# Performance work log

Hardware: AMD Instinct MI355X
Metric: run time of the kernel (lower is better)

The kernel has to match this reference:

```python
import jax, jax.numpy as jnp
import numpy as np

N = 50000      # nodes
E = 800000     # edges (before self-loops)
NFEAT = 128
NHID = 32
H = 8
NCLASS = 47
NEG_SLOPE = 0.2  # PyG GATv2Conv default


def gatv2_layer(x, src, dst, Wl, Wr, att, b, n):
    """One GATv2Conv layer (concat over heads). att: [H, C]."""
    h, c = att.shape
    xl = (x @ Wl).reshape(n, h, c)  # source transform (lin_l)
    xr = (x @ Wr).reshape(n, h, c)  # target transform (lin_r)
    e = jax.nn.leaky_relu(xl[src] + xr[dst], NEG_SLOPE)   # [E, H, C]
    logits = jnp.einsum('ehc,hc->eh', e, att)             # [E, H]
    # segment softmax over incoming edges of each target node
    m = jax.ops.segment_max(logits, dst, num_segments=n)  # [N, H]
    alpha = jnp.exp(logits - m[dst])
    denom = jax.ops.segment_sum(alpha, dst, num_segments=n)
    alpha = alpha / (denom[dst] + 1e-16)
    msg = xl[src] * alpha[:, :, None]                     # [E, H, C]
    out = jax.ops.segment_sum(msg, dst, num_segments=n)   # [N, H, C]
    return out.reshape(n, h * c) + b


def setup_inputs():
    key = jax.random.key(0)
    ks = jax.random.split(key, 16)
    s = 0.1
    x = jax.random.normal(ks[0], (N, NFEAT), jnp.float32)
    edge_index = jax.random.randint(ks[1], (2, E), 0, N)
    HID = H * NHID  # 256
    params = dict(
        Wl0=jax.random.normal(ks[2], (NFEAT, HID), jnp.float32) * s,
        Wr0=jax.random.normal(ks[3], (NFEAT, HID), jnp.float32) * s,
        a0=jax.random.normal(ks[4], (H, NHID), jnp.float32) * s,
        b0=jnp.zeros((HID,), jnp.float32),
        Wl1=jax.random.normal(ks[5], (HID, HID), jnp.float32) * s,
        Wr1=jax.random.normal(ks[6], (HID, HID), jnp.float32) * s,
        a1=jax.random.normal(ks[7], (H, NHID), jnp.float32) * s,
        b1=jnp.zeros((HID,), jnp.float32),
        Wl2=jax.random.normal(ks[8], (HID, NCLASS), jnp.float32) * s,
        Wr2=jax.random.normal(ks[9], (HID, NCLASS), jnp.float32) * s,
        a2=jax.random.normal(ks[10], (1, NCLASS), jnp.float32) * s,
        b2=jnp.zeros((NCLASS,), jnp.float32),
    )
    return {"x": x, "edge_index": edge_index, **params}


def reference(x, edge_index, Wl0, Wr0, a0, b0, Wl1, Wr1, a1, b1, Wl2, Wr2, a2, b2):
    n = x.shape[0]
    # PyG GATv2Conv adds self-loops by default
    loops = jnp.arange(n, dtype=edge_index.dtype)
    src = jnp.concatenate([edge_index[0], loops])
    dst = jnp.concatenate([edge_index[1], loops])
    h = gatv2_layer(x, src, dst, Wl0, Wr0, a0, b0, n)
    h = jax.nn.elu(h)
    h = gatv2_layer(h, src, dst, Wl1, Wr1, a1, b1, n)
    h = jax.nn.elu(h)
    h = gatv2_layer(h, src, dst, Wl2, Wr2, a2, b2, n)
    return jax.nn.log_softmax(h, axis=-1)
```

## Files before the change

kernel.cpp:

```cpp
#include <hip/hip_runtime.h>
#include <cmath>


#define NFEAT 128
#define HID 256
#define NCLS 47
#define L2PAD 64

typedef __attribute__((ext_vector_type(8))) short bf16x8;
typedef __attribute__((ext_vector_type(4))) float f32x4;
typedef __attribute__((ext_vector_type(2))) float f32x2;

__device__ __forceinline__ unsigned short f2b(float f) {
  unsigned int u = __builtin_bit_cast(unsigned int, f);
  u += 0x7FFFu + ((u >> 16) & 1u);
  return (unsigned short)(u >> 16);
}
__device__ __forceinline__ float b2f(unsigned short s) {
  return __builtin_bit_cast(float, (unsigned int)s << 16);
}
__device__ __forceinline__ f32x2 b2f2(unsigned int u) {
  return (f32x2){__builtin_bit_cast(float, u << 16),
                 __builtin_bit_cast(float, u & 0xFFFF0000u)};
}

__device__ __forceinline__ void glds16(const unsigned short* g, unsigned short* l) {
  __builtin_amdgcn_global_load_lds(
      (const __attribute__((address_space(1))) unsigned int*)g,
      (__attribute__((address_space(3))) unsigned int*)l, 16, 0, 0);
}

__global__ void k_cast_bf16(const float* __restrict__ in,
                            unsigned short* __restrict__ out, int n4) {
  int i = blockIdx.x * blockDim.x + threadIdx.x;
  if (i < n4) {
    float4 v = reinterpret_cast<const float4*>(in)[i];
    ushort4 o = {f2b(v.x), f2b(v.y), f2b(v.z), f2b(v.w)};
    reinterpret_cast<ushort4*>(out)[i] = o;
  }
}

struct WtArgs {
  const float* W[6];
  unsigned short* WT[6];
  int K[6], M[6], off[6], total;
};
__global__ void k_wt_all(WtArgs a) {
  int i = blockIdx.x * blockDim.x + threadIdx.x;
  if (i >= a.total) return;
  int s = 0;
  #pragma unroll
  for (int j = 1; j < 6; ++j) if (i >= a.off[j]) s = j;
  int jj = i - a.off[s];
  int K = a.K[s], M = a.M[s];
  int m = jj / K, k = jj - m * K;
  a.WT[s][jj] = (m < M) ? f2b(a.W[s][(size_t)k * M + m]) : (unsigned short)0;
}

__global__ void k_pad_att(const float* __restrict__ a, float* __restrict__ out48) {
  int i = threadIdx.x;
  if (i < 48) out48[i] = (i < NCLS) ? a[i] : 0.f;
}

__global__ void k_init_deg(int* __restrict__ deg, int n) {
  int i = blockIdx.x * blockDim.x + threadIdx.x;
  if (i < n) deg[i] = 1;
}

__global__ void k_count(const int* __restrict__ dst, int* __restrict__ deg, int e) {
  int i = blockIdx.x * blockDim.x + threadIdx.x;
  if (i < e) atomicAdd(&deg[dst[i]], 1);
}

__global__ __launch_bounds__(256) void k_bsum(const int* __restrict__ deg,
                                              int* __restrict__ bsum, int n) {
  int t = threadIdx.x;
  int base = blockIdx.x * 1024 + t * 4;
  int s = 0;
  if (base + 3 < n) {
    int4 v = *reinterpret_cast<const int4*>(deg + base);
    s = v.x + v.y + v.z + v.w;
  } else {
    for (int j = 0; j < 4; ++j) { int i = base + j; if (i < n) s += deg[i]; }
  }
  #pragma unroll
  for (int off = 1; off < 64; off <<= 1) s += __shfl_xor(s, off, 64);
  __shared__ int wsum[4];
  if ((t & 63) == 0) wsum[t >> 6] = s;
  __syncthreads();
  if (t == 0) bsum[blockIdx.x] = wsum[0] + wsum[1] + wsum[2] + wsum[3];
}

__global__ void k_scanb(int* __restrict__ bsum, int nb) {
  int lane = threadIdx.x;
  int v = (lane < nb) ? bsum[lane] : 0;
  #pragma unroll
  for (int off = 1; off < 64; off <<= 1) {
    int u = __shfl_up(v, off, 64);
    if (lane >= off) v += u;
  }
  if (lane < nb) bsum[lane] = v;
}

__global__ __launch_bounds__(256) void k_scanfinal(const int* __restrict__ deg,
                                                   const int* __restrict__ bscan,
                                                   int* __restrict__ rowptr, int n) {
  int t = threadIdx.x, b = blockIdx.x;
  int base = b * 1024 + t * 4;
  int v0 = 0, v1 = 0, v2 = 0, v3 = 0;
  if (base + 3 < n) {
    int4 v = *reinterpret_cast<const int4*>(deg + base);
    v0 = v.x; v1 = v.y; v2 = v.z; v3 = v.w;
  } else {
    if (base < n) v0 = deg[base];
    if (base + 1 < n) v1 = deg[base + 1];
    if (base + 2 < n) v2 = deg[base + 2];
    if (base + 3 < n) v3 = deg[base + 3];
  }
  int s = v0 + v1 + v2 + v3;
  int incl = s;
  #pragma unroll
  for (int off = 1; off < 64; off <<= 1) {
    int u = __shfl_up(incl, off, 64);
    if ((t & 63) >= off) incl += u;
  }
  __shared__ int wsum[4];
  int w = t >> 6, l = t & 63;
  if (l == 63) wsum[w] = incl;
  __syncthreads();
  int woff = 0;
  for (int j = 0; j < w; ++j) woff += wsum[j];
  int excl = incl - s + woff;
  int boff = (b == 0) ? 0 : bscan[b - 1];
  int p = boff + excl;
  if (base < n)     rowptr[base + 1] = p + v0;
  if (base + 1 < n) rowptr[base + 2] = p + v0 + v1;
  if (base + 2 < n) rowptr[base + 3] = p + v0 + v1 + v2;
  if (base + 3 < n) rowptr[base + 4] = p + v0 + v1 + v2 + v3;
  if (b == 0 && t == 0) rowptr[0] = 0;
}

__global__ void k_init_csr(const int* __restrict__ rowptr, int* __restrict__ adj,
                           int* __restrict__ vdst, int* __restrict__ cursor, int n) {
  int i = blockIdx.x * blockDim.x + threadIdx.x;
  if (i < n) { int p = rowptr[i]; adj[p] = i; vdst[p] = i; cursor[i] = p + 1; }
}

__global__ void k_scatter(const int* __restrict__ src, const int* __restrict__ dst,
                          int* __restrict__ cursor, int* __restrict__ adj,
                          int* __restrict__ vdst, int e) {
  int i = blockIdx.x * blockDim.x + threadIdx.x;
  if (i < e) {
    int d = dst[i];
    int p = atomicAdd(&cursor[d], 1);
    adj[p] = src[i];
    vdst[p] = d;
  }
}

__global__ __launch_bounds__(256) void gemm_dual_bf16(
    const unsigned short* __restrict__ X, const unsigned short* __restrict__ WlT,
    const unsigned short* __restrict__ WrT, unsigned short* __restrict__ XL,
    unsigned short* __restrict__ XR, int N, int K, int Mpad) {
  __shared__ __align__(16) unsigned short S[3 * 64 * 64];
  unsigned short* Xs = S;
  unsigned short* Ls = S + 4096;
  unsigned short* Rs = S + 8192;

  const int t = threadIdx.x;
  const int col0 = blockIdx.x * 64;
  const int row0 = blockIdx.y * 64;
  const int w = t >> 6, lane = t & 63;
  const int r15 = lane & 15, kc = lane >> 4;
  const bool tail = (row0 + 64 > N);

  const int rowa = t >> 3, c16a = t & 7;
  const int rowb = (t + 256) >> 3, c16b = t & 7;
  const int sga = (c16a ^ (rowa & 7)) * 8;
  const int sgb = (c16b ^ (rowb & 7)) * 8;
  unsigned short* ldst0 = S + (w * 512);
  unsigned short* ldst1 = S + (2048 + w * 512);

  f32x4 accL[4], accR[4];
  #pragma unroll
  for (int i = 0; i < 4; ++i) {
    accL[i] = (f32x4){0.f, 0.f, 0.f, 0.f};
    accR[i] = (f32x4){0.f, 0.f, 0.f, 0.f};
  }

  const int rA = 16 * w + r15;

  for (int k0 = 0; k0 < K; k0 += 64) {
    glds16(WlT + (size_t)(col0 + rowa) * K + k0 + sga, ldst0 + 4096);
    glds16(WlT + (size_t)(col0 + rowb) * K + k0 + sgb, ldst1 + 4096);
    glds16(WrT + (size_t)(col0 + rowa) * K + k0 + sga, ldst0 + 8192);
    glds16(WrT + (size_t)(col0 + rowb) * K + k0 + sgb, ldst1 + 8192);
    if (!tail) {
      glds16(X + (size_t)(row0 + rowa) * K + k0 + sga, ldst0);
      glds16(X + (size_t)(row0 + rowb) * K + k0 + sgb, ldst1);
    } else {
      uint4 va = (uint4){0, 0, 0, 0}, vb = (uint4){0, 0, 0, 0};
      if (row0 + rowa < N)
        va = *reinterpret_cast<const uint4*>(X + (size_t)(row0 + rowa) * K + k0 + sga);
      if (row0 + rowb < N)
        vb = *reinterpret_cast<const uint4*>(X + (size_t)(row0 + rowb) * K + k0 + sgb);
      *reinterpret_cast<uint4*>(Xs + rowa * 64 + c16a * 8) = va;
      *reinterpret_cast<uint4*>(Xs + rowb * 64 + c16b * 8) = vb;
    }
    __syncthreads();

    #pragma unroll
    for (int ks = 0; ks < 2; ++ks) {
      const int c16 = ks * 4 + kc;
      const bf16x8 a = *reinterpret_cast<const bf16x8*>(
          Xs + rA * 64 + ((c16 ^ (rA & 7)) * 8));
      #pragma unroll
      for (int nf = 0; nf < 4; ++nf) {
        const int rB = nf * 16 + r15;
        const int so = rB * 64 + ((c16 ^ (rB & 7)) * 8);
        const bf16x8 bl = *reinterpret_cast<const bf16x8*>(Ls + so);
        const bf16x8 br = *reinterpret_cast<const bf16x8*>(Rs + so);
        accL[nf] = __builtin_amdgcn_mfma_f32_16x16x32_bf16(a, bl, accL[nf], 0, 0, 0);
        accR[nf] = __builtin_amdgcn_mfma_f32_16x16x32_bf16(a, br, accR[nf], 0, 0, 0);
      }
    }
    __syncthreads();
  }

  #pragma unroll
  for (int nf = 0; nf < 4; ++nf) {
    int cc = col0 + nf * 16 + r15;
    #pragma unroll
    for (int i = 0; i < 4; ++i) {
      int rr = row0 + 16 * w + kc * 4 + i;
      if (rr < N) {
        XL[(size_t)rr * Mpad + cc] = f2b(accL[nf][i]);
        XR[(size_t)rr * Mpad + cc] = f2b(accR[nf][i]);
      }
    }
  }
}

__global__ __launch_bounds__(256) void gat_node_hc(
    const unsigned short* __restrict__ xl, const unsigned short* __restrict__ xr,
    const float* __restrict__ att, const float* __restrict__ bias,
    const int* __restrict__ rowptr, const int* __restrict__ adj,
    unsigned short* __restrict__ out, int n) {
  int wid = (blockIdx.x * blockDim.x + threadIdx.x) >> 6;
  int lane = threadIdx.x & 63;
  if (wid >= n) return;
  const int q = lane & 31, half = lane >> 5;

  const uint4 xrp = *reinterpret_cast<const uint4*>(xr + (size_t)wid * HID + q * 8);
  const f32x2 xr2[4] = {b2f2(xrp.x), b2f2(xrp.y), b2f2(xrp.z), b2f2(xrp.w)};
  const float4 af0 = *reinterpret_cast<const float4*>(att + q * 8);
  const float4 af1 = *reinterpret_cast<const float4*>(att + q * 8 + 4);
  const f32x2 a2[4] = {{af0.x, af0.y}, {af0.z, af0.w},
                       {af1.x, af1.y}, {af1.z, af1.w}};

  float m = -1e30f, denom = 0.f;
  f32x2 acc[4] = {{0.f, 0.f}, {0.f, 0.f}, {0.f, 0.f}, {0.f, 0.f}};

  const int beg = rowptr[wid], end = rowptr[wid + 1];
  for (int base = beg; base < end; base += 4) {
    const int e0 = base + half, e1 = base + 2 + half;
    const bool act0 = e0 < end, act1 = e1 < end;
    const int u0 = adj[act0 ? e0 : beg];
    const int u1 = adj[act1 ? e1 : beg];
    const uint4 p0 = *reinterpret_cast<const uint4*>(xl + (size_t)u0 * HID + q * 8);
    const uint4 p1 = *reinterpret_cast<const uint4*>(xl + (size_t)u1 * HID + q * 8);
    const f32x2 x0[4] = {b2f2(p0.x), b2f2(p0.y), b2f2(p0.z), b2f2(p0.w)};
    const f32x2 x1[4] = {b2f2(p1.x), b2f2(p1.y), b2f2(p1.z), b2f2(p1.w)};
    float part0, part1;
    {
      f32x2 s2 = {0.f, 0.f};
      #pragma unroll
      for (int j = 0; j < 4; ++j) {
        f32x2 z = x0[j] + xr2[j];
        f32x2 lz = 0.2f * z;
        f32x2 r = {fmaxf(z.x, lz.x), fmaxf(z.y, lz.y)};
        s2 += r * a2[j];
      }
      part0 = s2.x + s2.y;
      part0 += __shfl_xor(part0, 1, 64);
      part0 += __shfl_xor(part0, 2, 64);
      if (!act0) part0 = -1e30f;
    }
    {
      f32x2 s2 = {0.f, 0.f};
      #pragma unroll
      for (int j = 0; j < 4; ++j) {
        f32x2 z = x1[j] + xr2[j];
        f32x2 lz = 0.2f * z;
        f32x2 r = {fmaxf(z.x, lz.x), fmaxf(z.y, lz.y)};
        s2 += r * a2[j];
      }
      part1 = s2.x + s2.y;
      part1 += __shfl_xor(part1, 1, 64);
      part1 += __shfl_xor(part1, 2, 64);
      if (!act1) part1 = -1e30f;
    }
    if (__any(fmaxf(part0, part1) > m + 8.f)) {
      {
        float mn = fmaxf(m, part0);
        float so = __expf(m - mn);
        float wn = act0 ? __expf(part0 - mn) : 0.f;
        denom = denom * so + wn;
        #pragma unroll
        for (int j = 0; j < 4; ++j) acc[j] = acc[j] * so + wn * x0[j];
        m = mn;
      }
      {
        float mn = fmaxf(m, part1);
        float so = __expf(m - mn);
        float wn = act1 ? __expf(part1 - mn) : 0.f;
        denom = denom * so + wn;
        #pragma unroll
        for (int j = 0; j < 4; ++j) acc[j] = acc[j] * so + wn * x1[j];
        m = mn;
      }
    } else {
      float w0 = act0 ? __expf(part0 - m) : 0.f;
      float w1 = act1 ? __expf(part1 - m) : 0.f;
      denom += w0 + w1;
      #pragma unroll
      for (int j = 0; j < 4; ++j) acc[j] += w0 * x0[j] + w1 * x1[j];
    }
  }

  float mo = __shfl_xor(m, 32, 64);
  float ms = fmaxf(m, mo);
  float sc = __expf(m - ms);
  denom *= sc;
  denom += __shfl_xor(denom, 32, 64);
  #pragma unroll
  for (int j = 0; j < 4; ++j) {
    acc[j] *= sc;
    acc[j].x += __shfl_xor(acc[j].x, 32, 64);
    acc[j].y += __shfl_xor(acc[j].y, 32, 64);
  }

  if (half == 0) {
    const float inv = 1.f / (denom + 1e-16f);
    const float4 bf0 = *reinterpret_cast<const float4*>(bias + q * 8);
    const float4 bf1 = *reinterpret_cast<const float4*>(bias + q * 8 + 4);
    float o[8] = {acc[0].x * inv + bf0.x, acc[0].y * inv + bf0.y,
                  acc[1].x * inv + bf0.z, acc[1].y * inv + bf0.w,
                  acc[2].x * inv + bf1.x, acc[2].y * inv + bf1.y,
                  acc[3].x * inv + bf1.z, acc[3].y * inv + bf1.w};
    #pragma unroll
    for (int j = 0; j < 8; ++j) o[j] = o[j] > 0.f ? o[j] : (__expf(o[j]) - 1.f);
    uint4 ov;
    ov.x = (unsigned)f2b(o[0]) | ((unsigned)f2b(o[1]) << 16);
    ov.y = (unsigned)f2b(o[2]) | ((unsigned)f2b(o[3]) << 16);
    ov.z = (unsigned)f2b(o[4]) | ((unsigned)f2b(o[5]) << 16);
    ov.w = (unsigned)f2b(o[6]) | ((unsigned)f2b(o[7]) << 16);
    *reinterpret_cast<uint4*>(out + (size_t)wid * HID + q * 8) = ov;
  }
}

__global__ __launch_bounds__(256) void k_logit_l2(
    const unsigned short* __restrict__ xl, const unsigned short* __restrict__ xr,
    const float* __restrict__ att48, const int* __restrict__ adj,
    const int* __restrict__ vdst, float* __restrict__ logit, int total) {
  int i = blockIdx.x * blockDim.x + threadIdx.x;
  if (i >= total) return;
  const int u = adj[i], v = vdst[i];
  const uint4* pu = reinterpret_cast<const uint4*>(xl + (size_t)u * L2PAD);
  const uint4* pv = reinterpret_cast<const uint4*>(xr + (size_t)v * L2PAD);
  f32x2 s2 = {0.f, 0.f};
  #pragma unroll
  for (int b = 0; b < 6; ++b) {
    const uint4 xu = pu[b], xv = pv[b];
    const f32x2* a2 = reinterpret_cast<const f32x2*>(att48 + b * 8);
    const unsigned ua[4] = {xu.x, xu.y, xu.z, xu.w};
    const unsigned va[4] = {xv.x, xv.y, xv.z, xv.w};
    #pragma unroll
    for (int j = 0; j < 4; ++j) {
      f32x2 z = b2f2(ua[j]) + b2f2(va[j]);
      f32x2 lz = 0.2f * z;
      f32x2 r = {fmaxf(z.x, lz.x), fmaxf(z.y, lz.y)};
      s2 += r * a2[j];
    }
  }
  logit[i] = s2.x + s2.y;
}

__global__ __launch_bounds__(256) void gat_node_l2(
    const unsigned short* __restrict__ xl, const float* __restrict__ logit,
    const float* __restrict__ bias, const int* __restrict__ rowptr,
    const int* __restrict__ adj, float* __restrict__ out, int n) {
  int wid = (blockIdx.x * blockDim.x + threadIdx.x) >> 6;
  int lane = threadIdx.x & 63;
  if (wid >= n) return;
  const bool act = lane < NCLS;
  const int beg = rowptr[wid], end = rowptr[wid + 1];

  float mx = -1e30f;
  for (int i = beg + lane; i < end; i += 64) mx = fmaxf(mx, logit[i]);
  #pragma unroll
  for (int off = 1; off < 64; off <<= 1) mx = fmaxf(mx, __shfl_xor(mx, off, 64));

  float denom = 0.f, acc = 0.f;
  int i = beg;
  for (; i + 1 < end; i += 2) {
    int u0 = adj[i], u1 = adj[i + 1];
    float w0 = __expf(logit[i] - mx);
    float w1 = __expf(logit[i + 1] - mx);
    float x0 = act ? b2f(xl[(size_t)u0 * L2PAD + lane]) : 0.f;
    float x1 = act ? b2f(xl[(size_t)u1 * L2PAD + lane]) : 0.f;
    denom += w0 + w1;
    acc += w0 * x0 + w1 * x1;
  }
  if (i < end) {
    int u0 = adj[i];
    float w0 = __expf(logit[i] - mx);
    float x0 = act ? b2f(xl[(size_t)u0 * L2PAD + lane]) : 0.f;
    denom += w0;
    acc += w0 * x0;
  }

  float r = acc / (denom + 1e-16f) + (act ? bias[lane] : 0.f);
  float rm = act ? r : -1e30f;
  #pragma unroll
  for (int off = 1; off < 64; off <<= 1) rm = fmaxf(rm, __shfl_xor(rm, off, 64));
  float se = act ? __expf(r - rm) : 0.f;
  #pragma unroll
  for (int off = 1; off < 64; off <<= 1) se += __shfl_xor(se, off, 64);
  if (act) out[(size_t)wid * NCLS + lane] = r - rm - __logf(se);
}

extern "C" void kernel_launch(void* const* d_in, const int* in_sizes, int n_in,
                              void* d_out, int out_size, void* d_ws, size_t ws_size,
                              hipStream_t stream) {
  const float* x   = (const float*)d_in[0];
  const int* ei    = (const int*)d_in[1];
  const float* Wl0 = (const float*)d_in[2];
  const float* Wr0 = (const float*)d_in[3];
  const float* a0  = (const float*)d_in[4];
  const float* b0  = (const float*)d_in[5];
  const float* Wl1 = (const float*)d_in[6];
  const float* Wr1 = (const float*)d_in[7];
  const float* a1  = (const float*)d_in[8];
  const float* b1  = (const float*)d_in[9];
  const float* Wl2 = (const float*)d_in[10];
  const float* Wr2 = (const float*)d_in[11];
  const float* a2  = (const float*)d_in[12];
  const float* b2  = (const float*)d_in[13];

  const int N = in_sizes[0] / NFEAT;
  const int E = in_sizes[1] / 2;
  const int* src = ei;
  const int* dst = ei + E;
  const int total = E + N;

  char* ws = (char*)d_ws;
  unsigned short* xlb = (unsigned short*)ws; ws += (size_t)N * HID * 2;
  unsigned short* xrb = (unsigned short*)ws; ws += (size_t)N * HID * 2;
  unsigned short* xb  = (unsigned short*)ws; ws += (size_t)N * HID * 2;
  unsigned short* hb  = (unsigned short*)ws; ws += (size_t)N * HID * 2;
  unsigned short* WT  = (unsigned short*)ws; ws += (size_t)6 * HID * HID * 2;
  float* logit = (float*)ws; ws += (size_t)total * sizeof(float);
  float* att48 = (float*)ws; ws += 64 * sizeof(float);
  int* deg    = (int*)ws; ws += (size_t)N * sizeof(int);
  int* rowptr = (int*)ws; ws += (size_t)(N + 8) * sizeof(int);
  int* bsum   = (int*)ws; ws += (size_t)64 * sizeof(int);
  int* adj    = (int*)ws; ws += (size_t)total * sizeof(int);
  int* vdst   = (int*)ws; ws += (size_t)total * sizeof(int);

  unsigned short* WlT0 = WT + 0 * HID * HID;
  unsigned short* WrT0 = WT + 1 * HID * HID;
  unsigned short* WlT1 = WT + 2 * HID * HID;
  unsigned short* WrT1 = WT + 3 * HID * HID;
  unsigned short* WlT2 = WT + 4 * HID * HID;
  unsigned short* WrT2 = WT + 5 * HID * HID;

  const int TB = 256;
  const int nbScan = (N + 1023) / 1024;

  k_cast_bf16<<<(N * NFEAT / 4 + TB - 1) / TB, TB, 0, stream>>>(x, xb, N * NFEAT / 4);
  {
    WtArgs a;
    const float* Wsrc[6] = {Wl0, Wr0, Wl1, Wr1, Wl2, Wr2};
    unsigned short* Wdst[6] = {WlT0, WrT0, WlT1, WrT1, WlT2, WrT2};
    int Ks[6] = {NFEAT, NFEAT, HID, HID, HID, HID};
    int Ms[6] = {HID, HID, HID, HID, NCLS, NCLS};
    int Mp[6] = {HID, HID, HID, HID, L2PAD, L2PAD};
    int off = 0;
    for (int s = 0; s < 6; ++s) {
      a.W[s] = Wsrc[s]; a.WT[s] = Wdst[s]; a.K[s] = Ks[s]; a.M[s] = Ms[s];
      a.off[s] = off; off += Mp[s] * Ks[s];
    }
    a.total = off;
    k_wt_all<<<(a.total + TB - 1) / TB, TB, 0, stream>>>(a);
  }
  k_pad_att<<<1, 64, 0, stream>>>(a2, att48);

  k_init_deg<<<(N + TB - 1) / TB, TB, 0, stream>>>(deg, N);
  k_count<<<(E + TB - 1) / TB, TB, 0, stream>>>(dst, deg, E);
  k_bsum<<<nbScan, TB, 0, stream>>>(deg, bsum, N);
  k_scanb<<<1, 64, 0, stream>>>(bsum, nbScan);
  k_scanfinal<<<nbScan, TB, 0, stream>>>(deg, bsum, rowptr, N);
  k_init_csr<<<(N + TB - 1) / TB, TB, 0, stream>>>(rowptr, adj, vdst, deg, N);
  k_scatter<<<(E + TB - 1) / TB, TB, 0, stream>>>(src, dst, deg, adj, vdst, E);

  const int nodeBlocks = (N + 3) / 4;
  const int rowBlocks = (N + 63) / 64;

  {
    dim3 g(HID / 64, rowBlocks);
    gemm_dual_bf16<<<g, 256, 0, stream>>>(xb, WlT0, WrT0, xlb, xrb, N, NFEAT, HID);
    gat_node_hc<<<nodeBlocks, 256, 0, stream>>>(xlb, xrb, a0, b0, rowptr, adj, hb, N);
  }
  {
    dim3 g(HID / 64, rowBlocks);
    gemm_dual_bf16<<<g, 256, 0, stream>>>(hb, WlT1, WrT1, xlb, xrb, N, HID, HID);
    gat_node_hc<<<nodeBlocks, 256, 0, stream>>>(xlb, xrb, a1, b1, rowptr, adj, xb, N);
  }
  {
    dim3 g(1, rowBlocks);
    gemm_dual_bf16<<<g, 256, 0, stream>>>(xb, WlT2, WrT2, xlb, xrb, N, HID, L2PAD);
    k_logit_l2<<<(total + TB - 1) / TB, TB, 0, stream>>>(xlb, xrb, att48, adj,
                                                         vdst, logit, total);
    gat_node_l2<<<nodeBlocks, 256, 0, stream>>>(xlb, logit, b2, rowptr, adj,
                                                (float*)d_out, N);
  }
}
```

Baseline: 425.7 us.

## Use 128x128 dual GEMM tiles, fuse small setup kernels, switch softmax to exp2

Adds a 512-thread GEMM with 128x128 tiles for the two 256-wide layers, so each X tile is reused across more output columns. The attention-padding kernel is folded into the weight-transpose kernel and CSR self-loop initialization into the final scan kernel, removing two launches. The node softmax is rewritten to handle one edge per half-wave per iteration, with attention pre-scaled by log2(e) so exp2f can be used; the rescale threshold is adjusted to match the base-2 scale. This trades ILP in the edge loop for simpler code, and the larger GEMM tile may reduce occupancy.

After: 431.9 us. No clear change (+1.5%).

```diff
diff --git a/kernel.cpp b/kernel.cpp
--- a/kernel.cpp
+++ b/kernel.cpp
@@ -6,6 +6,7 @@
 #define HID 256
 #define NCLS 47
 #define L2PAD 64
+#define LOG2E 1.44269504088896340736f
 
 typedef __attribute__((ext_vector_type(8))) short bf16x8;
 typedef __attribute__((ext_vector_type(4))) float f32x4;
@@ -23,7 +24,6 @@
   return (f32x2){__builtin_bit_cast(float, u << 16),
                  __builtin_bit_cast(float, u & 0xFFFF0000u)};
 }
-
 __device__ __forceinline__ void glds16(const unsigned short* g, unsigned short* l) {
   __builtin_amdgcn_global_load_lds(
       (const __attribute__((address_space(1))) unsigned int*)g,
@@ -44,10 +44,16 @@
   const float* W[6];
   unsigned short* WT[6];
   int K[6], M[6], off[6], total;
+  const float* att;
+  float* att48;
 };
 __global__ void k_wt_all(WtArgs a) {
   int i = blockIdx.x * blockDim.x + threadIdx.x;
-  if (i >= a.total) return;
+  if (i >= a.total) {
+    int j = i - a.total;
+    if (j < 48) a.att48[j] = (j < NCLS) ? a.att[j] * LOG2E : 0.f;
+    return;
+  }
   int s = 0;
   #pragma unroll
   for (int j = 1; j < 6; ++j) if (i >= a.off[j]) s = j;
@@ -55,11 +61,6 @@
   int K = a.K[s], M = a.M[s];
   int m = jj / K, k = jj - m * K;
   a.WT[s][jj] = (m < M) ? f2b(a.W[s][(size_t)k * M + m]) : (unsigned short)0;
-}
-
-__global__ void k_pad_att(const float* __restrict__ a, float* __restrict__ out48) {
-  int i = threadIdx.x;
-  if (i < 48) out48[i] = (i < NCLS) ? a[i] : 0.f;
 }
 
 __global__ void k_init_deg(int* __restrict__ deg, int n) {
@@ -104,7 +105,10 @@
 
 __global__ __launch_bounds__(256) void k_scanfinal(const int* __restrict__ deg,
                                                    const int* __restrict__ bscan,
-                                                   int* __restrict__ rowptr, int n) {
+                                                   int* __restrict__ rowptr,
+                                                   int* __restrict__ adj,
+                                                   int* __restrict__ vdst,
+                                                   int* __restrict__ cursor, int n) {
   int t = threadIdx.x, b = blockIdx.x;
   int base = b * 1024 + t * 4;
   int v0 = 0, v1 = 0, v2 = 0, v3 = 0;
@@ -132,18 +136,13 @@
   for (int j = 0; j < w; ++j) woff += wsum[j];
   int excl = incl - s + woff;
   int boff = (b == 0) ? 0 : bscan[b - 1];
-  int p = boff + excl;
-  if (base < n)     rowptr[base + 1] = p + v0;
-  if (base + 1 < n) rowptr[base + 2] = p + v0 + v1;
-  if (base + 2 < n) rowptr[base + 3] = p + v0 + v1 + v2;
-  if (base + 3 < n) rowptr[base + 4] = p + v0 + v1 + v2 + v3;
+  int p0 = boff + excl;
+  int p1 = p0 + v0, p2 = p1 + v1, p3 = p2 + v2, p4 = p3 + v3;
+  if (base < n)     { rowptr[base + 1] = p1; adj[p0] = base;     vdst[p0] = base;     cursor[base]     = p0 + 1; }
+  if (base + 1 < n) { rowptr[base + 2] = p2; adj[p1] = base + 1; vdst[p1] = base + 1; cursor[base + 1] = p1 + 1; }
+  if (base + 2 < n) { rowptr[base + 3] = p3; adj[p2] = base + 2; vdst[p2] = base + 2; cursor[base + 2] = p2 + 1; }
+  if (base + 3 < n) { rowptr[base + 4] = p4; adj[p3] = base + 3; vdst[p3] = base + 3; cursor[base + 3] = p3 + 1; }
   if (b == 0 && t == 0) rowptr[0] = 0;
-}
-
-__global__ void k_init_csr(const int* __restrict__ rowptr, int* __restrict__ adj,
-                           int* __restrict__ vdst, int* __restrict__ cursor, int n) {
-  int i = blockIdx.x * blockDim.x + threadIdx.x;
-  if (i < n) { int p = rowptr[i]; adj[p] = i; vdst[p] = i; cursor[i] = p + 1; }
 }
 
 __global__ void k_scatter(const int* __restrict__ src, const int* __restrict__ dst,
@@ -155,6 +154,100 @@
     int p = atomicAdd(&cursor[d], 1);
     adj[p] = src[i];
     vdst[p] = d;
+  }
+}
+
+__global__ __launch_bounds__(512) void gemm_dual_bf16_128(
+    const unsigned short* __restrict__ X, const unsigned short* __restrict__ WlT,
+    const unsigned short* __restrict__ WrT, unsigned short* __restrict__ XL,
+    unsigned short* __restrict__ XR, int N, int K, int Mpad) {
+  __shared__ __align__(16) unsigned short S[3 * 128 * 64];
+  unsigned short* Xs = S;
+  unsigned short* Ls = S + 8192;
+  unsigned short* Rs = S + 16384;
+
+  const int t = threadIdx.x;
+  const int col0 = blockIdx.x * 128;
+  const int row0 = blockIdx.y * 128;
+  const int w = t >> 6, lane = t & 63;
+  const int wr = w >> 2, wc = w & 3;
+  const int r15 = lane & 15, kc = lane >> 4;
+  const bool tail = (row0 + 128 > N);
+
+  const int row_a = t >> 3,          c16_a = t & 7;
+  const int row_b = (t + 512) >> 3,  c16_b = t & 7;
+  const int sg_a = (c16_a ^ (row_a & 7)) * 8;
+  const int sg_b = (c16_b ^ (row_b & 7)) * 8;
+  unsigned short* d0 = S + w * 512;
+  unsigned short* d1 = S + 4096 + w * 512;
+
+  f32x4 accL[4][2], accR[4][2];
+  #pragma unroll
+  for (int rf = 0; rf < 4; ++rf)
+    #pragma unroll
+    for (int cf = 0; cf < 2; ++cf) {
+      accL[rf][cf] = (f32x4){0.f, 0.f, 0.f, 0.f};
+      accR[rf][cf] = (f32x4){0.f, 0.f, 0.f, 0.f};
+    }
+
+  for (int k0 = 0; k0 < K; k0 += 64) {
+    glds16(WlT + (size_t)(col0 + row_a) * K + k0 + sg_a, d0 + 8192);
+    glds16(WlT + (size_t)(col0 + row_b) * K + k0 + sg_b, d1 + 8192);
+    glds16(WrT + (size_t)(col0 + row_a) * K + k0 + sg_a, d0 + 16384);
+    glds16(WrT + (size_t)(col0 + row_b) * K + k0 + sg_b, d1 + 16384);
+    if (!tail) {
+      glds16(X + (size_t)(row0 + row_a) * K + k0 + sg_a, d0);
+      glds16(X + (size_t)(row0 + row_b) * K + k0 + sg_b, d1);
+    } else {
+      uint4 va = (uint4){0, 0, 0, 0}, vb = (uint4){0, 0, 0, 0};
+      if (row0 + row_a < N)
+        va = *reinterpret_cast<const uint4*>(X + (size_t)(row0 + row_a) * K + k0 + sg_a);
+      if (row0 + row_b < N)
+        vb = *reinterpret_cast<const uint4*>(X + (size_t)(row0 + row_b) * K + k0 + sg_b);
+      *reinterpret_cast<uint4*>(Xs + row_a * 64 + c16_a * 8) = va;
+      *reinterpret_cast<uint4*>(Xs + row_b * 64 + c16_b * 8) = vb;
+    }
+    __syncthreads();
+
+    #pragma unroll
+    for (int ks = 0; ks < 2; ++ks) {
+      const int c16 = ks * 4 + kc;
+      bf16x8 a[4];
+      #pragma unroll
+      for (int rf = 0; rf < 4; ++rf) {
+        const int rA = wr * 64 + rf * 16 + r15;
+        a[rf] = *reinterpret_cast<const bf16x8*>(Xs + rA * 64 + ((c16 ^ (rA & 7)) * 8));
+      }
+      #pragma unroll
+      for (int cf = 0; cf < 2; ++cf) {
+        const int rB = wc * 32 + cf * 16 + r15;
+        const int so = rB * 64 + ((c16 ^ (rB & 7)) * 8);
+        const bf16x8 bl = *reinterpret_cast<const bf16x8*>(Ls + so);
+        const bf16x8 br = *reinterpret_cast<const bf16x8*>(Rs + so);
+        #pragma unroll
+        for (int rf = 0; rf < 4; ++rf) {
+          accL[rf][cf] = __builtin_amdgcn_mfma_f32_16x16x32_bf16(a[rf], bl, accL[rf][cf], 0, 0, 0);
+          accR[rf][cf] = __builtin_amdgcn_mfma_f32_16x16x32_bf16(a[rf], br, accR[rf][cf], 0, 0, 0);
+        }
+      }
+    }
+    __syncthreads();
+  }
+
+  #pragma unroll
+  for (int rf = 0; rf < 4; ++rf) {
+    #pragma unroll
+    for (int cf = 0; cf < 2; ++cf) {
+      int cc = col0 + wc * 32 + cf * 16 + r15;
+      #pragma unroll
+      for (int i = 0; i < 4; ++i) {
+        int rr = row0 + wr * 64 + rf * 16 + kc * 4 + i;
+        if (rr < N) {
+          XL[(size_t)rr * Mpad + cc] = f2b(accL[rf][cf][i]);
+          XR[(size_t)rr * Mpad + cc] = f2b(accR[rf][cf][i]);
+        }
+      }
+    }
   }
 }
 
@@ -255,82 +348,50 @@
   const f32x2 xr2[4] = {b2f2(xrp.x), b2f2(xrp.y), b2f2(xrp.z), b2f2(xrp.w)};
   const float4 af0 = *reinterpret_cast<const float4*>(att + q * 8);
   const float4 af1 = *reinterpret_cast<const float4*>(att + q * 8 + 4);
-  const f32x2 a2[4] = {{af0.x, af0.y}, {af0.z, af0.w},
-                       {af1.x, af1.y}, {af1.z, af1.w}};
+  const f32x2 a2[4] = {{af0.x * LOG2E, af0.y * LOG2E}, {af0.z * LOG2E, af0.w * LOG2E},
+                       {af1.x * LOG2E, af1.y * LOG2E}, {af1.z * LOG2E, af1.w * LOG2E}};
 
   float m = -1e30f, denom = 0.f;
   f32x2 acc[4] = {{0.f, 0.f}, {0.f, 0.f}, {0.f, 0.f}, {0.f, 0.f}};
 
   const int beg = rowptr[wid], end = rowptr[wid + 1];
-  for (int base = beg; base < end; base += 4) {
-    const int e0 = base + half, e1 = base + 2 + half;
-    const bool act0 = e0 < end, act1 = e1 < end;
-    const int u0 = adj[act0 ? e0 : beg];
-    const int u1 = adj[act1 ? e1 : beg];
-    const uint4 p0 = *reinterpret_cast<const uint4*>(xl + (size_t)u0 * HID + q * 8);
-    const uint4 p1 = *reinterpret_cast<const uint4*>(xl + (size_t)u1 * HID + q * 8);
-    const f32x2 x0[4] = {b2f2(p0.x), b2f2(p0.y), b2f2(p0.z), b2f2(p0.w)};
-    const f32x2 x1[4] = {b2f2(p1.x), b2f2(p1.y), b2f2(p1.z), b2f2(p1.w)};
-    float part0, part1;
-    {
-      f32x2 s2 = {0.f, 0.f};
+  for (int base = beg; base < end; base += 2) {
+    const int i = base + half;
+    const bool act = i < end;
+    const int u = adj[act ? i : base];
+    const uint4 p = *reinterpret_cast<const uint4*>(xl + (size_t)u * HID + q * 8);
+    const f32x2 x2[4] = {b2f2(p.x), b2f2(p.y), b2f2(p.z), b2f2(p.w)};
+    f32x2 s2 = {0.f, 0.f};
+    #pragma unroll
+    for (int j = 0; j < 4; ++j) {
+      f32x2 z = x2[j] + xr2[j];
+      f32x2 lz = 0.2f * z;
+      f32x2 r = {fmaxf(z.x, lz.x), fmaxf(z.y, lz.y)};
+      s2 += r * a2[j];
+    }
+    float part = s2.x + s2.y;
+    part += __shfl_xor(part, 1, 64);
+    part += __shfl_xor(part, 2, 64);
+    if (!act) part = -1e30f;
+    if (__any(part > m + 11.54f)) {
+      float mn = fmaxf(m, part);
+      float so = exp2f(m - mn);
+      float wn = act ? exp2f(part - mn) : 0.f;
+      denom = denom * so + wn;
       #pragma unroll
-      for (int j = 0; j < 4; ++j) {
-        f32x2 z = x0[j] + xr2[j];
-        f32x2 lz = 0.2f * z;
-        f32x2 r = {fmaxf(z.x, lz.x), fmaxf(z.y, lz.y)};
-        s2 += r * a2[j];
-      }
-      part0 = s2.x + s2.y;
-      part0 += __shfl_xor(part0, 1, 64);
-      part0 += __shfl_xor(part0, 2, 64);
-      if (!act0) part0 = -1e30f;
-    }
-    {
-      f32x2 s2 = {0.f, 0.f};
+      for (int j = 0; j < 4; ++j) acc[j] = acc[j] * so + wn * x2[j];
+      m = mn;
+    } else {
+      float wn = act ? exp2f(part - m) : 0.f;
+      denom += wn;
       #pragma unroll
-      for (int j = 0; j < 4; ++j) {
-        f32x2 z = x1[j] + xr2[j];
-        f32x2 lz = 0.2f * z;
-        f32x2 r = {fmaxf(z.x, lz.x), fmaxf(z.y, lz.y)};
-        s2 += r * a2[j];
-      }
-      part1 = s2.x + s2.y;
-      part1 += __shfl_xor(part1, 1, 64);
-      part1 += __shfl_xor(part1, 2, 64);
-      if (!act1) part1 = -1e30f;
-    }
-    if (__any(fmaxf(part0, part1) > m + 8.f)) {
-      {
-        float mn = fmaxf(m, part0);
-        float so = __expf(m - mn);
-        float wn = act0 ? __expf(part0 - mn) : 0.f;
-        denom = denom * so + wn;
-        #pragma unroll
-        for (int j = 0; j < 4; ++j) acc[j] = acc[j] * so + wn * x0[j];
-        m = mn;
-      }
-      {
-        float mn = fmaxf(m, part1);
-        float so = __expf(m - mn);
-        float wn = act1 ? __expf(part1 - mn) : 0.f;
-        denom = denom * so + wn;
-        #pragma unroll
-        for (int j = 0; j < 4; ++j) acc[j] = acc[j] * so + wn * x1[j];
-        m = mn;
-      }
-    } else {
-      float w0 = act0 ? __expf(part0 - m) : 0.f;
-      float w1 = act1 ? __expf(part1 - m) : 0.f;
-      denom += w0 + w1;
-      #pragma unroll
-      for (int j = 0; j < 4; ++j) acc[j] += w0 * x0[j] + w1 * x1[j];
+      for (int j = 0; j < 4; ++j) acc[j] += wn * x2[j];
     }
   }
 
   float mo = __shfl_xor(m, 32, 64);
   float ms = fmaxf(m, mo);
-  float sc = __expf(m - ms);
+  float sc = exp2f(m - ms);
   denom *= sc;
   denom += __shfl_xor(denom, 32, 64);
   #pragma unroll
@@ -405,8 +466,8 @@
   int i = beg;
   for (; i + 1 < end; i += 2) {
     int u0 = adj[i], u1 = adj[i + 1];
-    float w0 = __expf(logit[i] - mx);
-    float w1 = __expf(logit[i + 1] - mx);
+    float w0 = exp2f(logit[i] - mx);
+    float w1 = exp2f(logit[i + 1] - mx);
     float x0 = act ? b2f(xl[(size_t)u0 * L2PAD + lane]) : 0.f;
     float x1 = act ? b2f(xl[(size_t)u1 * L2PAD + lane]) : 0.f;
     denom += w0 + w1;
@@ -414,7 +475,7 @@
   }
   if (i < end) {
     int u0 = adj[i];
-    float w0 = __expf(logit[i] - mx);
+    float w0 = exp2f(logit[i] - mx);
     float x0 = act ? b2f(xl[(size_t)u0 * L2PAD + lane]) : 0.f;
     denom += w0;
     acc += w0 * x0;
@@ -492,33 +553,33 @@
       a.off[s] = off; off += Mp[s] * Ks[s];
     }
     a.total = off;
-    k_wt_all<<<(a.total + TB - 1) / TB, TB, 0, stream>>>(a);
-  }
-  k_pad_att<<<1, 64, 0, stream>>>(a2, att48);
+    a.att = a2; a.att48 = att48;
+    k_wt_all<<<(a.total + 48 + TB - 1) / TB, TB, 0, stream>>>(a);
+  }
 
   k_init_deg<<<(N + TB - 1) / TB, TB, 0, stream>>>(deg, N);
   k_count<<<(E + TB - 1) / TB, TB, 0, stream>>>(dst, deg, E);
   k_bsum<<<nbScan, TB, 0, stream>>>(deg, bsum, N);
   k_scanb<<<1, 64, 0, stream>>>(bsum, nbScan);
-  k_scanfinal<<<nbScan, TB, 0, stream>>>(deg, bsum, rowptr, N);
-  k_init_csr<<<(N + TB - 1) / TB, TB, 0, stream>>>(rowptr, adj, vdst, deg, N);
+  k_scanfinal<<<nbScan, TB, 0, stream>>>(deg, bsum, rowptr, adj, vdst, deg, N);
   k_scatter<<<(E + TB - 1) / TB, TB, 0, stream>>>(src, dst, deg, adj, vdst, E);
 
   const int nodeBlocks = (N + 3) / 4;
-  const int rowBlocks = (N + 63) / 64;
+  const int rb128 = (N + 127) / 128;
+  const int rb64 = (N + 63) / 64;
 
   {
-    dim3 g(HID / 64, rowBlocks);
-    gemm_dual_bf16<<<g, 256, 0, stream>>>(xb, WlT0, WrT0, xlb, xrb, N, NFEAT, HID);
+    dim3 g(HID / 128, rb128);
+    gemm_dual_bf16_128<<<g, 512, 0, stream>>>(xb, WlT0, WrT0, xlb, xrb, N, NFEAT, HID);
     gat_node_hc<<<nodeBlocks, 256, 0, stream>>>(xlb, xrb, a0, b0, rowptr, adj, hb, N);
   }
   {
-    dim3 g(HID / 64, rowBlocks);
-    gemm_dual_bf16<<<g, 256, 0, stream>>>(hb, WlT1, WrT1, xlb, xrb, N, HID, HID);
+    dim3 g(HID / 128, rb128);
+    gemm_dual_bf16_128<<<g, 512, 0, stream>>>(hb, WlT1, WrT1, xlb, xrb, N, HID, HID);
     gat_node_hc<<<nodeBlocks, 256, 0, stream>>>(xlb, xrb, a1, b1, rowptr, adj, xb, N);
   }
   {
-    dim3 g(1, rowBlocks);
+    dim3 g(1, rb64);
     gemm_dual_bf16<<<g, 256, 0, stream>>>(xb, WlT2, WrT2, xlb, xrb, N, HID, L2PAD);
     k_logit_l2<<<(total + TB - 1) / TB, TB, 0, stream>>>(xlb, xrb, att48, adj,
                                                          vdst, logit, total);
```
